# Kernel optimization log

Hardware: AMD Instinct MI355X
Metric: run time of the kernel (lower is better)

## Reference

```python
import jax, jax.numpy as jnp
import numpy as np

N_UNITS, HASH, BASIS = 32, 1024, 128
C, H, W = 3, 64, 64
D = C * H * W  # 12288
B = 16
DEPTH = 16


def setup_inputs() -> dict:
    key = jax.random.key(0)
    k0, k1, k2, k3, k4 = jax.random.split(key, 5)
    x = jax.random.normal(k0, (B, C, H, W), dtype=jnp.float32)
    P = jax.random.normal(k1, (D, HASH), dtype=jnp.float32) / np.float32(np.sqrt(D))
    basis = jax.random.normal(k2, (N_UNITS, HASH, BASIS), dtype=jnp.float32) / np.float32(np.sqrt(HASH))
    Wt = jax.random.normal(k3, (D, D), dtype=jnp.float32) / np.float32(np.sqrt(D))
    b = jax.random.normal(k4, (N_UNITS, D), dtype=jnp.float32) * 0.01
    return {"x": x, "P": P, "basis": basis, "Wt": Wt, "b": b, "depth": DEPTH}


def reference(x, P, basis, Wt, b, depth):
    """HRN routing, inference mode (all units populated).

    Returns (hashes (B, hash_feat), routes (B, depth) int32).
    """
    Bn = x.shape[0]
    n_units, hash_feat, _ = basis.shape
    xf_all = x.reshape(Bn, -1)  # (B, D)

    def one_exemplar(xf0):
        h0 = xf0 @ P  # (HASH,) hash of the exemplar
        mask0 = jnp.ones((n_units,), dtype=bool)  # units still available
        out0 = jnp.zeros((hash_feat,), dtype=xf0.dtype)

        def step(carry, _):
            xf, h, mask, out = carry
            # projection of h onto every unit's basis: (h @ B_u) @ B_u^T
            coeff = jnp.einsum('f,ufk->uk', h, basis)
            proj = jnp.einsum('uk,ufk->uf', coeff, basis)  # (n_units, HASH)
            mags = jnp.sqrt(jnp.sum(proj * proj, axis=-1))
            mags = jnp.where(mask, mags, -jnp.inf)
            idx = jnp.argmax(mags)  # routed unit
            residual = h - proj[idx]
            out = out + residual
            mask = mask.at[idx].set(False)
            # selected unit transforms the exemplar and re-hashes
            xf2 = jnp.tanh(xf @ Wt + b[idx])
            h2 = xf2 @ P
            return (xf2, h2, mask, out), idx.astype(jnp.int32)

        (_, _, _, out), route = jax.lax.scan(step, (xf0, h0, mask0, out0), None, length=depth)
        return out, route

    hashes, routes = jax.vmap(one_exemplar)(xf_all)
    return hashes, routes
```

## Files before the change

### kernel.cpp

```cpp
#include <hip/hip_runtime.h>
#include <math.h>

#define NU     32
#define HASHF  1024
#define BASISK 128
#define DD     12288
#define BN     16
#define DEPTH  16

#define KC_Y   32
#define KCH_Y  384
#define KC_H   64
#define KCH_H  192

__global__ __launch_bounds__(256) void k_transpose(const float* __restrict__ x,
                                                   float* __restrict__ xfT) {
    int i = blockIdx.x * 256 + threadIdx.x;
    int b = i / DD, k = i % DD;
    xfT[(size_t)k * BN + b] = x[i];
}

__global__ __launch_bounds__(128) void k_S(const float* __restrict__ basis,
                                           float* __restrict__ S) {
    int u  = blockIdx.x >> 3;
    int it = blockIdx.x & 7;
    int t  = threadIdx.x;
    int i0 = it * 16;

    __shared__ float lrow[8 * BASISK];
    float acc[16];
#pragma unroll
    for (int i = 0; i < 16; i++) acc[i] = 0.f;

    const float* bu = basis + (size_t)u * HASHF * BASISK;
    for (int fb = 0; fb < HASHF / 8; fb++) {
#pragma unroll
        for (int r = 0; r < 8; r++)
            lrow[r * BASISK + t] = bu[(size_t)(fb * 8 + r) * BASISK + t];
        __syncthreads();
#pragma unroll
        for (int r = 0; r < 8; r++) {
            float wj = lrow[r * BASISK + t];
#pragma unroll
            for (int i = 0; i < 16; i++)
                acc[i] += lrow[r * BASISK + i0 + i] * wj;
        }
        __syncthreads();
    }
#pragma unroll
    for (int i = 0; i < 16; i++)
        S[((size_t)u * BASISK + i0 + i) * BASISK + t] = acc[i];
}

__global__ __launch_bounds__(256) void k_big(const float* __restrict__ xfT,
                                             const float* __restrict__ Wt,
                                             float* __restrict__ y_part,
                                             const float* __restrict__ h_part,
                                             const float* __restrict__ basis,
                                             float* __restrict__ coeff_part) {
    __shared__ float smem[KCH_Y * BN];
    int t = threadIdx.x;

    if (blockIdx.x < 128) {
        int u2 = blockIdx.x >> 3;
        int fc = blockIdx.x & 7;
        int u  = u2 * 2 + (t >> 7);
        int k  = t & 127;

        for (int j = t; j < 128 * BN; j += 256) {
            int fl = j >> 4, b = j & 15;
            float s = 0.f;
            const float* hp = h_part + (size_t)(fc * 128 + fl) * BN + b;
#pragma unroll 4
            for (int c = 0; c < KC_H; c++) s += hp[(size_t)c * (HASHF * BN)];
            smem[fl * BN + b] = s;
        }
        __syncthreads();

        float acc[BN];
#pragma unroll
        for (int b = 0; b < BN; b++) acc[b] = 0.f;
        const float* bp = basis + ((size_t)u * HASHF + fc * 128) * BASISK + k;
        for (int fl = 0; fl < 128; fl++) {
            float w = bp[(size_t)fl * BASISK];
            const float4* lv = (const float4*)&smem[fl * BN];
#pragma unroll
            for (int q = 0; q < 4; q++) {
                float4 a = lv[q];
                acc[4*q+0] += a.x * w;
                acc[4*q+1] += a.y * w;
                acc[4*q+2] += a.z * w;
                acc[4*q+3] += a.w * w;
            }
        }
#pragma unroll
        for (int b = 0; b < BN; b++)
            coeff_part[((size_t)(fc * BN + b) * NU + u) * BASISK + k] = acc[b];
    } else {
        int m  = blockIdx.x - 128;
        int nt = m % 24;
        int c  = m / 24;
        int n0 = nt * 512 + t * 2;
        int kbase = c * KCH_Y;

        for (int j = t; j < KCH_Y * BN; j += 256)
            smem[j] = xfT[(size_t)kbase * BN + j];
        __syncthreads();

        float2 acc[BN];
#pragma unroll
        for (int b = 0; b < BN; b++) acc[b] = make_float2(0.f, 0.f);

        const float* wp = Wt + (size_t)kbase * DD + n0;
        for (int kl = 0; kl < KCH_Y; kl += 8) {
            float2 w[8];
#pragma unroll
            for (int r = 0; r < 8; r++)
                w[r] = *(const float2*)(wp + (size_t)(kl + r) * DD);
#pragma unroll
            for (int r = 0; r < 8; r++) {
                const float4* xv = (const float4*)&smem[(kl + r) * BN];
#pragma unroll
                for (int q = 0; q < 4; q++) {
                    float4 a = xv[q];
                    acc[4*q+0].x += a.x * w[r].x; acc[4*q+0].y += a.x * w[r].y;
                    acc[4*q+1].x += a.y * w[r].x; acc[4*q+1].y += a.y * w[r].y;
                    acc[4*q+2].x += a.z * w[r].x; acc[4*q+2].y += a.z * w[r].y;
                    acc[4*q+3].x += a.w * w[r].x; acc[4*q+3].y += a.w * w[r].y;
                }
            }
        }
#pragma unroll
        for (int b = 0; b < BN; b++)
            *(float2*)&y_part[(size_t)c * (BN * DD) + (size_t)b * DD + n0] = acc[b];
    }
}

__global__ __launch_bounds__(128) void k_mags(const float* __restrict__ coeff_part,
                                              const float* __restrict__ S,
                                              float* __restrict__ coeff_full,
                                              float* __restrict__ mags) {
    int b = blockIdx.x >> 5;
    int u = blockIdx.x & 31;
    int t = threadIdx.x;

    __shared__ float lc[BASISK];
    __shared__ float red[BASISK];

    float cv = 0.f;
#pragma unroll
    for (int fc = 0; fc < 8; fc++)
        cv += coeff_part[((size_t)(fc * BN + b) * NU + u) * BASISK + t];
    lc[t] = cv;
    coeff_full[((size_t)b * NU + u) * BASISK + t] = cv;
    __syncthreads();

    float v = 0.f;
    const float* Sp = S + (size_t)u * BASISK * BASISK + t;
#pragma unroll 4
    for (int i = 0; i < BASISK; i++) v += Sp[(size_t)i * BASISK] * lc[i];

    red[t] = v * cv;
    __syncthreads();
    for (int s = 64; s > 0; s >>= 1) {
        if (t < s) red[t] += red[t + s];
        __syncthreads();
    }
    if (t == 0) mags[b * NU + u] = red[0];
}

__global__ __launch_bounds__(128) void k_resid(const float* __restrict__ mags,
                                               const float* __restrict__ coeff_full,
                                               const float* __restrict__ basis,
                                               const float* __restrict__ h_part,
                                               float* __restrict__ out_acc,
                                               int* __restrict__ routes, int s) {
    int b  = blockIdx.x >> 3;
    int fc = blockIdx.x & 7;
    int t  = threadIdx.x;

    __shared__ int sel_s;
    __shared__ float lc[BASISK];
    if (t == 0) {
        unsigned mask = 0xFFFFFFFFu;
        for (int j = 0; j < s; j++) mask &= ~(1u << routes[b * DEPTH + j]);
        float best = -1.f; int bi = 0;
        for (int u = 0; u < NU; u++) {
            if (mask & (1u << u)) {
                float m = mags[b * NU + u];
                if (m > best) { best = m; bi = u; }
            }
        }
        sel_s = bi;
        if (fc == 0) routes[b * DEPTH + s] = bi;
    }
    __syncthreads();
    int u = sel_s;
    lc[t] = coeff_full[((size_t)b * NU + u) * BASISK + t];
    __syncthreads();

    int f = fc * 128 + t;
    float hv = 0.f;
    const float* hp = h_part + (size_t)f * BN + b;
#pragma unroll 4
    for (int c = 0; c < KC_H; c++) hv += hp[(size_t)c * (HASHF * BN)];

    const float4* br = (const float4*)&basis[((size_t)u * HASHF + f) * BASISK];
    const float4* cr = (const float4*)lc;
    float dot = 0.f;
#pragma unroll
    for (int j = 0; j < 32; j++) {
        float4 bv = br[j], c4 = cr[j];
        dot += bv.x * c4.x + bv.y * c4.y + bv.z * c4.z + bv.w * c4.w;
    }
    out_acc[b * HASHF + f] += hv - dot;
}

__global__ __launch_bounds__(256) void k_ytanh(const float* __restrict__ y_part,
                                               const float* __restrict__ bias,
                                               const int* __restrict__ routes,
                                               float* __restrict__ xfT_next, int s) {
    int i = blockIdx.x * 256 + threadIdx.x;
    int b = i / DD, n = i % DD;
    float sum = 0.f;
#pragma unroll 4
    for (int c = 0; c < KC_Y; c++) sum += y_part[(size_t)c * (BN * DD) + i];
    int u = routes[b * DEPTH + s];
    float v = tanhf(sum + bias[(size_t)u * DD + n]);
    xfT_next[(size_t)n * BN + b] = v;
}

__global__ __launch_bounds__(256) void k_matP(const float* __restrict__ xfT,
                                              const float* __restrict__ P,
                                              float* __restrict__ h_part) {
    int nt = blockIdx.x & 1;
    int c  = blockIdx.x >> 1;
    int t  = threadIdx.x;
    int f0 = nt * 512 + t * 2;
    int kbase = c * KCH_H;

    __shared__ float lxf[KCH_H * BN];
    for (int j = t; j < KCH_H * BN; j += 256)
        lxf[j] = xfT[(size_t)kbase * BN + j];
    __syncthreads();

    float2 acc[BN];
#pragma unroll
    for (int b = 0; b < BN; b++) acc[b] = make_float2(0.f, 0.f);

    const float* wp = P + (size_t)kbase * HASHF + f0;
    for (int kl = 0; kl < KCH_H; kl += 8) {
        float2 w[8];
#pragma unroll
        for (int r = 0; r < 8; r++)
            w[r] = *(const float2*)(wp + (size_t)(kl + r) * HASHF);
#pragma unroll
        for (int r = 0; r < 8; r++) {
            const float4* xv = (const float4*)&lxf[(kl + r) * BN];
#pragma unroll
            for (int q = 0; q < 4; q++) {
                float4 a = xv[q];
                acc[4*q+0].x += a.x * w[r].x; acc[4*q+0].y += a.x * w[r].y;
                acc[4*q+1].x += a.y * w[r].x; acc[4*q+1].y += a.y * w[r].y;
                acc[4*q+2].x += a.z * w[r].x; acc[4*q+2].y += a.z * w[r].y;
                acc[4*q+3].x += a.w * w[r].x; acc[4*q+3].y += a.w * w[r].y;
            }
        }
    }
    float* hp = h_part + (size_t)c * (HASHF * BN) + (size_t)f0 * BN;
#pragma unroll
    for (int fi = 0; fi < 2; fi++) {
#pragma unroll
        for (int q = 0; q < 4; q++) {
            float4 v;
            v.x = fi ? acc[4*q+0].y : acc[4*q+0].x;
            v.y = fi ? acc[4*q+1].y : acc[4*q+1].x;
            v.z = fi ? acc[4*q+2].y : acc[4*q+2].x;
            v.w = fi ? acc[4*q+3].y : acc[4*q+3].x;
            *(float4*)&hp[fi * BN + q * 4] = v;
        }
    }
}

__global__ __launch_bounds__(256) void k_out(const float* __restrict__ out_acc,
                                             const int* __restrict__ routes,
                                             float* __restrict__ o, int n) {
    int i = blockIdx.x * 256 + threadIdx.x;
    if (i >= n) return;
    if (i < BN * HASHF) o[i] = out_acc[i];
    else o[i] = (float)routes[i - BN * HASHF];
}

extern "C" void kernel_launch(void* const* d_in, const int* in_sizes, int n_in,
                              void* d_out, int out_size, void* d_ws, size_t ws_size,
                              hipStream_t stream) {
    const float* x     = (const float*)d_in[0];
    const float* P     = (const float*)d_in[1];
    const float* basis = (const float*)d_in[2];
    const float* Wt    = (const float*)d_in[3];
    const float* bias  = (const float*)d_in[4];
    float* out = (float*)d_out;

    float* w = (float*)d_ws;
    size_t off = 0;
    auto alloc = [&](size_t nf) { float* p = w + off; off += nf; return p; };

    float* xfT0       = alloc((size_t)DD * BN);
    float* xfT1       = alloc((size_t)DD * BN);
    float* out_acc    = alloc(BN * HASHF);
    float* coeff_part = alloc((size_t)8 * BN * NU * BASISK);
    float* coeff_full = alloc((size_t)BN * NU * BASISK);
    float* mags       = alloc(BN * NU);
    float* S          = alloc((size_t)NU * BASISK * BASISK);
    int*   routes     = (int*)alloc(BN * DEPTH);
    float* y_part     = alloc((size_t)KC_Y * BN * DD);
    float* h_part     = alloc((size_t)KC_H * BN * HASHF);
    (void)ws_size;

    hipMemsetAsync(out_acc, 0, BN * HASHF * sizeof(float), stream);

    k_transpose<<<(BN * DD) / 256, 256, 0, stream>>>(x, xfT0);
    k_S<<<NU * 8, 128, 0, stream>>>(basis, S);
    k_matP<<<2 * KC_H, 256, 0, stream>>>(xfT0, P, h_part);

    for (int s = 0; s < DEPTH; s++) {
        float* cur = (s & 1) ? xfT1 : xfT0;
        float* nxt = (s & 1) ? xfT0 : xfT1;

        k_big<<<128 + 24 * KC_Y, 256, 0, stream>>>(cur, Wt, y_part, h_part, basis, coeff_part);
        k_mags<<<BN * NU, 128, 0, stream>>>(coeff_part, S, coeff_full, mags);
        k_resid<<<BN * 8, 128, 0, stream>>>(mags, coeff_full, basis, h_part, out_acc, routes, s);
        k_ytanh<<<(BN * DD) / 256, 256, 0, stream>>>(y_part, bias, routes, nxt, s);
        if (s < DEPTH - 1)
            k_matP<<<2 * KC_H, 256, 0, stream>>>(nxt, P, h_part);
    }

    k_out<<<(BN * HASHF + BN * DEPTH + 255) / 256, 256, 0, stream>>>(out_acc, routes, out, out_size);
}
```

Before: 3.984 ms.

## Fuse argmax into mags via atomicMax and merge tanh, matP, residual into one tail kernel

Each depth step now runs three kernels instead of five. The argmax moves into the magnitude kernel through a packed 64-bit atomicMax key, so the separate selection kernel is gone. The tanh reduction is fused into the P-projection and residual work inside one tail kernel, and k_big writes the reduced hash once so the residual no longer re-sums the partials. It also skips already-used units, skips the Wt matmul and matP on the last step, and changes the P split to 128 chunks of 96. Each matP block recomputes the tanh for its K chunk (duplicated across two column blocks), adds a slot of atomics, and adds more partial sums to reduce.

```diff
diff --git a/kernel.cpp b/kernel.cpp
--- a/kernel.cpp
+++ b/kernel.cpp
@@ -10,8 +10,9 @@
 
 #define KC_Y   32
 #define KCH_Y  384
-#define KC_H   64
-#define KCH_H  192
+#define KC_H   128
+#define KCH_H  96
+#define LXF_LD 20
 
 __global__ __launch_bounds__(256) void k_transpose(const float* __restrict__ x,
                                                    float* __restrict__ xfT) {
@@ -52,12 +53,65 @@
         S[((size_t)u * BASISK + i0 + i) * BASISK + t] = acc[i];
 }
 
+__global__ __launch_bounds__(256) void k_matP(const float* __restrict__ xfT,
+                                              const float* __restrict__ P,
+                                              float* __restrict__ h_part) {
+    int nt = blockIdx.x & 1;
+    int c  = blockIdx.x >> 1;
+    int t  = threadIdx.x;
+    int f0 = nt * 512 + t * 2;
+    int kbase = c * KCH_H;
+
+    __shared__ float lxf[KCH_H * BN];
+    for (int j = t; j < KCH_H * BN; j += 256)
+        lxf[j] = xfT[(size_t)kbase * BN + j];
+    __syncthreads();
+
+    float2 acc[BN];
+#pragma unroll
+    for (int b = 0; b < BN; b++) acc[b] = make_float2(0.f, 0.f);
+
+    const float* wp = P + (size_t)kbase * HASHF + f0;
+    for (int kl = 0; kl < KCH_H; kl += 8) {
+        float2 w[8];
+#pragma unroll
+        for (int r = 0; r < 8; r++)
+            w[r] = *(const float2*)(wp + (size_t)(kl + r) * HASHF);
+#pragma unroll
+        for (int r = 0; r < 8; r++) {
+            const float4* xv = (const float4*)&lxf[(kl + r) * BN];
+#pragma unroll
+            for (int q = 0; q < 4; q++) {
+                float4 a = xv[q];
+                acc[4*q+0].x += a.x * w[r].x; acc[4*q+0].y += a.x * w[r].y;
+                acc[4*q+1].x += a.y * w[r].x; acc[4*q+1].y += a.y * w[r].y;
+                acc[4*q+2].x += a.z * w[r].x; acc[4*q+2].y += a.z * w[r].y;
+                acc[4*q+3].x += a.w * w[r].x; acc[4*q+3].y += a.w * w[r].y;
+            }
+        }
+    }
+    float* hp = h_part + (size_t)c * (HASHF * BN) + (size_t)f0 * BN;
+#pragma unroll
+    for (int fi = 0; fi < 2; fi++) {
+#pragma unroll
+        for (int q = 0; q < 4; q++) {
+            float4 v;
+            v.x = fi ? acc[4*q+0].y : acc[4*q+0].x;
+            v.y = fi ? acc[4*q+1].y : acc[4*q+1].x;
+            v.z = fi ? acc[4*q+2].y : acc[4*q+2].x;
+            v.w = fi ? acc[4*q+3].y : acc[4*q+3].x;
+            *(float4*)&hp[fi * BN + q * 4] = v;
+        }
+    }
+}
+
 __global__ __launch_bounds__(256) void k_big(const float* __restrict__ xfT,
                                              const float* __restrict__ Wt,
                                              float* __restrict__ y_part,
                                              const float* __restrict__ h_part,
                                              const float* __restrict__ basis,
-                                             float* __restrict__ coeff_part) {
+                                             float* __restrict__ coeff_part,
+                                             float* __restrict__ h_full) {
     __shared__ float smem[KCH_Y * BN];
     int t = threadIdx.x;
 
@@ -69,11 +123,12 @@
 
         for (int j = t; j < 128 * BN; j += 256) {
             int fl = j >> 4, b = j & 15;
-            float s = 0.f;
+            float sum = 0.f;
             const float* hp = h_part + (size_t)(fc * 128 + fl) * BN + b;
 #pragma unroll 4
-            for (int c = 0; c < KC_H; c++) s += hp[(size_t)c * (HASHF * BN)];
-            smem[fl * BN + b] = s;
+            for (int c = 0; c < KC_H; c++) sum += hp[(size_t)c * (HASHF * BN)];
+            smem[fl * BN + b] = sum;
+            if (u2 == 0) h_full[(size_t)(fc * 128 + fl) * BN + b] = sum;
         }
         __syncthreads();
 
@@ -136,16 +191,26 @@
     }
 }
 
-__global__ __launch_bounds__(128) void k_mags(const float* __restrict__ coeff_part,
-                                              const float* __restrict__ S,
-                                              float* __restrict__ coeff_full,
-                                              float* __restrict__ mags) {
+__global__ __launch_bounds__(128) void k_magsmax(const float* __restrict__ coeff_part,
+                                                 const float* __restrict__ S,
+                                                 float* __restrict__ coeff_full,
+                                                 unsigned long long* __restrict__ best,
+                                                 const int* __restrict__ routes, int s) {
     int b = blockIdx.x >> 5;
     int u = blockIdx.x & 31;
     int t = threadIdx.x;
 
+    __shared__ int s_used;
     __shared__ float lc[BASISK];
     __shared__ float red[BASISK];
+
+    if (t == 0) {
+        int used = 0;
+        for (int j = 0; j < s; j++) used |= (routes[b * DEPTH + j] == u);
+        s_used = used;
+    }
+    __syncthreads();
+    if (s_used) return;
 
     float cv = 0.f;
 #pragma unroll
@@ -157,128 +222,118 @@
 
     float v = 0.f;
     const float* Sp = S + (size_t)u * BASISK * BASISK + t;
-#pragma unroll 4
+#pragma unroll 8
     for (int i = 0; i < BASISK; i++) v += Sp[(size_t)i * BASISK] * lc[i];
 
     red[t] = v * cv;
     __syncthreads();
-    for (int s = 64; s > 0; s >>= 1) {
-        if (t < s) red[t] += red[t + s];
-        __syncthreads();
-    }
-    if (t == 0) mags[b * NU + u] = red[0];
-}
-
-__global__ __launch_bounds__(128) void k_resid(const float* __restrict__ mags,
-                                               const float* __restrict__ coeff_full,
-                                               const float* __restrict__ basis,
-                                               const float* __restrict__ h_part,
-                                               float* __restrict__ out_acc,
-                                               int* __restrict__ routes, int s) {
-    int b  = blockIdx.x >> 3;
-    int fc = blockIdx.x & 7;
-    int t  = threadIdx.x;
-
-    __shared__ int sel_s;
-    __shared__ float lc[BASISK];
+    for (int st = 64; st > 0; st >>= 1) {
+        if (t < st) red[t] += red[t + st];
+        __syncthreads();
+    }
     if (t == 0) {
-        unsigned mask = 0xFFFFFFFFu;
-        for (int j = 0; j < s; j++) mask &= ~(1u << routes[b * DEPTH + j]);
-        float best = -1.f; int bi = 0;
-        for (int u = 0; u < NU; u++) {
-            if (mask & (1u << u)) {
-                float m = mags[b * NU + u];
-                if (m > best) { best = m; bi = u; }
+        float mag = fmaxf(red[0], 0.f);
+        unsigned long long key =
+            ((unsigned long long)__float_as_uint(mag) << 6) |
+            (unsigned long long)(31 - u);
+        atomicMax(best + (size_t)s * BN + b, key);
+    }
+}
+
+__global__ __launch_bounds__(256) void k_tail(const float* __restrict__ y_part,
+                                              const float* __restrict__ bias,
+                                              const unsigned long long* __restrict__ best,
+                                              const float* __restrict__ P,
+                                              float* __restrict__ xfT_next,
+                                              float* __restrict__ h_part,
+                                              const float* __restrict__ h_full,
+                                              const float* __restrict__ coeff_full,
+                                              const float* __restrict__ basis,
+                                              float* __restrict__ out_acc,
+                                              int* __restrict__ routes,
+                                              int s, int nMatP) {
+    int t = threadIdx.x;
+
+    if ((int)blockIdx.x < nMatP) {
+        __shared__ float lxf[KCH_H * LXF_LD];
+        int nt = blockIdx.x & 1;
+        int c  = blockIdx.x >> 1;
+        int kbase = c * KCH_H;
+
+        for (int j = t; j < KCH_H * BN; j += 256) {
+            int b  = j / KCH_H;
+            int fl = j - b * KCH_H;
+            float sum = 0.f;
+            const float* yp = y_part + (size_t)b * DD + kbase + fl;
+#pragma unroll 4
+            for (int cc = 0; cc < KC_Y; cc++) sum += yp[(size_t)cc * (BN * DD)];
+            int u = 31 - (int)(best[(size_t)s * BN + b] & 63ull);
+            float v = tanhf(sum + bias[(size_t)u * DD + kbase + fl]);
+            lxf[fl * LXF_LD + b] = v;
+            if (nt == (fl >= KCH_H / 2 ? 1 : 0))
+                xfT_next[(size_t)(kbase + fl) * BN + b] = v;
+        }
+        __syncthreads();
+
+        int f0 = nt * 512 + t * 2;
+        float2 acc[BN];
+#pragma unroll
+        for (int b = 0; b < BN; b++) acc[b] = make_float2(0.f, 0.f);
+
+        const float* wp = P + (size_t)kbase * HASHF + f0;
+        for (int kl = 0; kl < KCH_H; kl += 8) {
+            float2 w[8];
+#pragma unroll
+            for (int r = 0; r < 8; r++)
+                w[r] = *(const float2*)(wp + (size_t)(kl + r) * HASHF);
+#pragma unroll
+            for (int r = 0; r < 8; r++) {
+                const float4* xv = (const float4*)&lxf[(kl + r) * LXF_LD];
+#pragma unroll
+                for (int q = 0; q < 4; q++) {
+                    float4 a = xv[q];
+                    acc[4*q+0].x += a.x * w[r].x; acc[4*q+0].y += a.x * w[r].y;
+                    acc[4*q+1].x += a.y * w[r].x; acc[4*q+1].y += a.y * w[r].y;
+                    acc[4*q+2].x += a.z * w[r].x; acc[4*q+2].y += a.z * w[r].y;
+                    acc[4*q+3].x += a.w * w[r].x; acc[4*q+3].y += a.w * w[r].y;
+                }
             }
         }
-        sel_s = bi;
-        if (fc == 0) routes[b * DEPTH + s] = bi;
-    }
-    __syncthreads();
-    int u = sel_s;
-    lc[t] = coeff_full[((size_t)b * NU + u) * BASISK + t];
-    __syncthreads();
-
-    int f = fc * 128 + t;
-    float hv = 0.f;
-    const float* hp = h_part + (size_t)f * BN + b;
-#pragma unroll 4
-    for (int c = 0; c < KC_H; c++) hv += hp[(size_t)c * (HASHF * BN)];
-
-    const float4* br = (const float4*)&basis[((size_t)u * HASHF + f) * BASISK];
-    const float4* cr = (const float4*)lc;
-    float dot = 0.f;
-#pragma unroll
-    for (int j = 0; j < 32; j++) {
-        float4 bv = br[j], c4 = cr[j];
-        dot += bv.x * c4.x + bv.y * c4.y + bv.z * c4.z + bv.w * c4.w;
-    }
-    out_acc[b * HASHF + f] += hv - dot;
-}
-
-__global__ __launch_bounds__(256) void k_ytanh(const float* __restrict__ y_part,
-                                               const float* __restrict__ bias,
-                                               const int* __restrict__ routes,
-                                               float* __restrict__ xfT_next, int s) {
-    int i = blockIdx.x * 256 + threadIdx.x;
-    int b = i / DD, n = i % DD;
-    float sum = 0.f;
-#pragma unroll 4
-    for (int c = 0; c < KC_Y; c++) sum += y_part[(size_t)c * (BN * DD) + i];
-    int u = routes[b * DEPTH + s];
-    float v = tanhf(sum + bias[(size_t)u * DD + n]);
-    xfT_next[(size_t)n * BN + b] = v;
-}
-
-__global__ __launch_bounds__(256) void k_matP(const float* __restrict__ xfT,
-                                              const float* __restrict__ P,
-                                              float* __restrict__ h_part) {
-    int nt = blockIdx.x & 1;
-    int c  = blockIdx.x >> 1;
-    int t  = threadIdx.x;
-    int f0 = nt * 512 + t * 2;
-    int kbase = c * KCH_H;
-
-    __shared__ float lxf[KCH_H * BN];
-    for (int j = t; j < KCH_H * BN; j += 256)
-        lxf[j] = xfT[(size_t)kbase * BN + j];
-    __syncthreads();
-
-    float2 acc[BN];
-#pragma unroll
-    for (int b = 0; b < BN; b++) acc[b] = make_float2(0.f, 0.f);
-
-    const float* wp = P + (size_t)kbase * HASHF + f0;
-    for (int kl = 0; kl < KCH_H; kl += 8) {
-        float2 w[8];
-#pragma unroll
-        for (int r = 0; r < 8; r++)
-            w[r] = *(const float2*)(wp + (size_t)(kl + r) * HASHF);
-#pragma unroll
-        for (int r = 0; r < 8; r++) {
-            const float4* xv = (const float4*)&lxf[(kl + r) * BN];
+        float* hp = h_part + (size_t)c * (HASHF * BN) + (size_t)f0 * BN;
+#pragma unroll
+        for (int fi = 0; fi < 2; fi++) {
 #pragma unroll
             for (int q = 0; q < 4; q++) {
-                float4 a = xv[q];
-                acc[4*q+0].x += a.x * w[r].x; acc[4*q+0].y += a.x * w[r].y;
-                acc[4*q+1].x += a.y * w[r].x; acc[4*q+1].y += a.y * w[r].y;
-                acc[4*q+2].x += a.z * w[r].x; acc[4*q+2].y += a.z * w[r].y;
-                acc[4*q+3].x += a.w * w[r].x; acc[4*q+3].y += a.w * w[r].y;
+                float4 v;
+                v.x = fi ? acc[4*q+0].y : acc[4*q+0].x;
+                v.y = fi ? acc[4*q+1].y : acc[4*q+1].x;
+                v.z = fi ? acc[4*q+2].y : acc[4*q+2].x;
+                v.w = fi ? acc[4*q+3].y : acc[4*q+3].x;
+                *(float4*)&hp[fi * BN + q * 4] = v;
             }
         }
-    }
-    float* hp = h_part + (size_t)c * (HASHF * BN) + (size_t)f0 * BN;
-#pragma unroll
-    for (int fi = 0; fi < 2; fi++) {
-#pragma unroll
-        for (int q = 0; q < 4; q++) {
-            float4 v;
-            v.x = fi ? acc[4*q+0].y : acc[4*q+0].x;
-            v.y = fi ? acc[4*q+1].y : acc[4*q+1].x;
-            v.z = fi ? acc[4*q+2].y : acc[4*q+2].x;
-            v.w = fi ? acc[4*q+3].y : acc[4*q+3].x;
-            *(float4*)&hp[fi * BN + q * 4] = v;
-        }
+    } else {
+        int rid = blockIdx.x - nMatP;
+        int b   = rid >> 2;
+        int fq  = rid & 3;
+        __shared__ float lc[BASISK];
+
+        int u = 31 - (int)(best[(size_t)s * BN + b] & 63ull);
+        if (t < BASISK) lc[t] = coeff_full[((size_t)b * NU + u) * BASISK + t];
+        if (t == 0 && fq == 0) routes[b * DEPTH + s] = u;
+        __syncthreads();
+
+        int f = fq * 256 + t;
+        float hv = h_full[(size_t)f * BN + b];
+        const float4* br = (const float4*)&basis[((size_t)u * HASHF + f) * BASISK];
+        const float4* cr = (const float4*)lc;
+        float dot = 0.f;
+#pragma unroll
+        for (int j = 0; j < 32; j++) {
+            float4 bv = br[j], c4 = cr[j];
+            dot += bv.x * c4.x + bv.y * c4.y + bv.z * c4.z + bv.w * c4.w;
+        }
+        out_acc[b * HASHF + f] += hv - dot;
     }
 }
 
@@ -308,16 +363,19 @@
     float* xfT0       = alloc((size_t)DD * BN);
     float* xfT1       = alloc((size_t)DD * BN);
     float* out_acc    = alloc(BN * HASHF);
+    unsigned long long* best = (unsigned long long*)alloc(DEPTH * BN * 2);
     float* coeff_part = alloc((size_t)8 * BN * NU * BASISK);
     float* coeff_full = alloc((size_t)BN * NU * BASISK);
-    float* mags       = alloc(BN * NU);
+    float* h_full     = alloc((size_t)HASHF * BN);
     float* S          = alloc((size_t)NU * BASISK * BASISK);
     int*   routes     = (int*)alloc(BN * DEPTH);
     float* y_part     = alloc((size_t)KC_Y * BN * DD);
     float* h_part     = alloc((size_t)KC_H * BN * HASHF);
     (void)ws_size;
 
-    hipMemsetAsync(out_acc, 0, BN * HASHF * sizeof(float), stream);
+    hipMemsetAsync(out_acc, 0,
+                   (size_t)BN * HASHF * sizeof(float) +
+                   (size_t)DEPTH * BN * sizeof(unsigned long long), stream);
 
     k_transpose<<<(BN * DD) / 256, 256, 0, stream>>>(x, xfT0);
     k_S<<<NU * 8, 128, 0, stream>>>(basis, S);
@@ -327,13 +385,17 @@
         float* cur = (s & 1) ? xfT1 : xfT0;
         float* nxt = (s & 1) ? xfT0 : xfT1;
 
-        k_big<<<128 + 24 * KC_Y, 256, 0, stream>>>(cur, Wt, y_part, h_part, basis, coeff_part);
-        k_mags<<<BN * NU, 128, 0, stream>>>(coeff_part, S, coeff_full, mags);
-        k_resid<<<BN * 8, 128, 0, stream>>>(mags, coeff_full, basis, h_part, out_acc, routes, s);
-        k_ytanh<<<(BN * DD) / 256, 256, 0, stream>>>(y_part, bias, routes, nxt, s);
-        if (s < DEPTH - 1)
-            k_matP<<<2 * KC_H, 256, 0, stream>>>(nxt, P, h_part);
-    }
-
-    k_out<<<(BN * HASHF + BN * DEPTH + 255) / 256, 256, 0, stream>>>(out_acc, routes, out, out_size);
-}
+        int nWt = (s < DEPTH - 1) ? 24 * KC_Y : 0;
+        k_big<<<128 + nWt, 256, 0, stream>>>(cur, Wt, y_part, h_part, basis,
+                                             coeff_part, h_full);
+        k_magsmax<<<BN * NU, 128, 0, stream>>>(coeff_part, S, coeff_full, best,
+                                               routes, s);
+        int nMatP = (s < DEPTH - 1) ? 2 * KC_H : 0;
+        k_tail<<<nMatP + 64, 256, 0, stream>>>(y_part, bias, best, P, nxt, h_part,
+                                               h_full, coeff_full, basis, out_acc,
+                                               routes, s, nMatP);
+    }
+
+    k_out<<<(BN * HASHF + BN * DEPTH + 255) / 256, 256, 0, stream>>>(out_acc, routes,
+                                                                     out, out_size);
+}
```

After: 4.477 ms. 12.4% more time.
